# Optimization experiments

Hardware: AMD Instinct MI355X
Metric: run time of the kernel (lower is better)

## Reference

```python
import jax, jax.numpy as jnp
import numpy as np

B, T = 32, 512
D_TOK, D_OH, D_DEP = 256, 32, 32
D = D_TOK + D_OH + D_DEP  # tree_input_size = 320
H = 64                    # tree_lstm_h_size
P, L, ROOT = 16384, 16, 8 # pairs, path length, root position on path
N = P * L
E = P * (L - 1)
NUM_LEVELS = 9            # max level = max(ROOT, L-1-ROOT) = 8 -> levels 0..8


def _structure():
    # Each subgraph is a shortest path in the dependency tree; edges on both
    # sides point toward the topological root (position ROOT).
    pos = np.arange(L)
    par = np.where(pos < ROOT, pos + 1, np.where(pos > ROOT, pos - 1, pos))
    base = (np.arange(P) * L)[:, None]
    parent_of = (base + par[None, :]).reshape(-1).astype(np.int32)
    nodes = (base + pos[None, :]).reshape(-1).astype(np.int32)
    is_root = np.tile(pos == ROOT, P)
    child = nodes[~is_root]
    parent = parent_of[~is_root]
    level_up = np.tile(np.where(pos <= ROOT, pos, L - 1 - pos), P).astype(np.int32)
    level_down = np.tile(np.abs(pos - ROOT), P).astype(np.int32)
    root_idx = (np.arange(P) * L + ROOT).astype(np.int32)
    start_idx = (np.arange(P) * L).astype(np.int32)
    end_idx = (np.arange(P) * L + (L - 1)).astype(np.int32)
    return child, parent, parent_of, level_up, level_down, root_idx, start_idx, end_idx


def setup_inputs() -> dict:
    key = jax.random.key(0)
    ks = jax.random.split(key, 24)
    sc = 0.02
    ch, pa, po, lu, ld, ri, si, ei = _structure()
    inp = {
        'token_embs': jax.random.normal(ks[0], (B, T, D_TOK), jnp.float32),
        'one_hot_embs': (jax.random.uniform(ks[1], (B, T, D_OH)) < 0.1).astype(jnp.float32),
        'dep_embs': jax.random.normal(ks[2], (B, T, D_DEP), jnp.float32),
        'node_b_idx': jax.random.randint(ks[3], (N,), 0, B, jnp.int32),
        'node_t_idx': jax.random.randint(ks[4], (N,), 0, T, jnp.int32),
        'child': jnp.asarray(ch), 'parent': jnp.asarray(pa),
        'parent_of': jnp.asarray(po),
        'level_up': jnp.asarray(lu), 'level_down': jnp.asarray(ld),
        'root_idx': jnp.asarray(ri), 'start_idx': jnp.asarray(si), 'end_idx': jnp.asarray(ei),
        # child-sum Tree-LSTM params, upward (bottom-up) direction
        'W_iou_up': jax.random.normal(ks[5], (D, 3 * H)) * sc,
        'U_iou_up': jax.random.normal(ks[6], (H, 3 * H)) * sc,
        'b_iou_up': jnp.zeros((3 * H,), jnp.float32),
        'W_f_up': jax.random.normal(ks[7], (D, H)) * sc,
        'U_f_up': jax.random.normal(ks[8], (H, H)) * sc,
        'b_f_up': jnp.zeros((H,), jnp.float32),
        # downward (top-down) direction
        'W_iou_dn': jax.random.normal(ks[9], (D, 3 * H)) * sc,
        'U_iou_dn': jax.random.normal(ks[10], (H, 3 * H)) * sc,
        'b_iou_dn': jnp.zeros((3 * H,), jnp.float32),
        'W_f_dn': jax.random.normal(ks[11], (D, H)) * sc,
        'U_f_dn': jax.random.normal(ks[12], (H, H)) * sc,
        'b_f_dn': jnp.zeros((H,), jnp.float32),
    }
    return inp


def _tree_lstm(x, child, parent, level, x_iou, x_f, U_iou, U_f):
    # Level-synchronous child-sum Tree-LSTM toward parents (bottom-up).
    n = x.shape[0]
    h0 = jnp.zeros((n, H), x.dtype)
    c0 = jnp.zeros((n, H), x.dtype)

    def step(carry, t):
        h, c = carry
        hs = jax.ops.segment_sum(h[child], parent, num_segments=n)          # sum child h
        f = jax.nn.sigmoid(x_f[parent] + h[child] @ U_f)                    # per-edge forget
        fc = jax.ops.segment_sum(f * c[child], parent, num_segments=n)
        i, o, u = jnp.split(x_iou + hs @ U_iou, 3, axis=-1)
        c_new = jax.nn.sigmoid(i) * jnp.tanh(u) + fc
        h_new = jax.nn.sigmoid(o) * jnp.tanh(c_new)
        m = (level == t)[:, None]
        return (jnp.where(m, h_new, h), jnp.where(m, c_new, c)), None

    (h, c), _ = jax.lax.scan(step, (h0, c0), jnp.arange(NUM_LEVELS))
    return h


def _tree_lstm_down(x, parent_of, level_down, x_iou, x_f, U_iou, U_f):
    # Top-down pass: each node has exactly one predecessor (its parent).
    n = x.shape[0]
    not_root = (level_down != 0).astype(x.dtype)[:, None]
    h0 = jnp.zeros((n, H), x.dtype)
    c0 = jnp.zeros((n, H), x.dtype)

    def step(carry, t):
        h, c = carry
        hp = h[parent_of] * not_root
        cp = c[parent_of] * not_root
        f = jax.nn.sigmoid(x_f + hp @ U_f)
        i, o, u = jnp.split(x_iou + hp @ U_iou, 3, axis=-1)
        c_new = jax.nn.sigmoid(i) * jnp.tanh(u) + f * cp
        h_new = jax.nn.sigmoid(o) * jnp.tanh(c_new)
        m = (level_down == t)[:, None]
        return (jnp.where(m, h_new, h), jnp.where(m, c_new, c)), None

    (h, c), _ = jax.lax.scan(step, (h0, c0), jnp.arange(NUM_LEVELS))
    return h


def reference(token_embs, one_hot_embs, dep_embs, node_b_idx, node_t_idx,
              child, parent, parent_of, level_up, level_down,
              root_idx, start_idx, end_idx,
              W_iou_up, U_iou_up, b_iou_up, W_f_up, U_f_up, b_f_up,
              W_iou_dn, U_iou_dn, b_iou_dn, W_f_dn, U_f_dn, b_f_dn):
    # node_embs = cat(token, one_hot, dep) gathered at subgraph node ids (_ID)
    full = jnp.concatenate((token_embs, one_hot_embs, dep_embs), axis=-1)  # [B,T,D]
    x = full[node_b_idx, node_t_idx]                                       # [N,D]

    # precompute input projections once
    xi_u = x @ W_iou_up + b_iou_up
    xf_u = x @ W_f_up + b_f_up
    xi_d = x @ W_iou_dn + b_iou_dn
    xf_d = x @ W_f_dn + b_f_dn

    h_up = _tree_lstm(x, child, parent, level_up, xi_u, xf_u, U_iou_up, U_f_up)
    h_dn = _tree_lstm_down(x, parent_of, level_down, xi_d, xf_d, U_iou_dn, U_f_dn)

    # tree_lstm_out.view(-1,2,H): slot 0 = bottom-up, slot 1 = top-down
    tree_pair_embs = jnp.concatenate(
        (h_up[root_idx], h_dn[start_idx], h_dn[end_idx]), axis=-1)          # [P, 3H]
    return tree_pair_embs
```

## Files before the change

### kernel.cpp

```cpp
#include <hip/hip_runtime.h>
#include <hip/hip_fp16.h>


typedef _Float16 f16x8 __attribute__((ext_vector_type(8)));
typedef _Float16 f16x4 __attribute__((ext_vector_type(4)));
typedef _Float16 f16x2 __attribute__((ext_vector_type(2)));
typedef float f32x4 __attribute__((ext_vector_type(4)));

#define NP 16
#define N2K 2.8853900817779268f

__device__ __forceinline__ void async16(const void* g, void* l) {
    __builtin_amdgcn_global_load_lds(
        (const __attribute__((address_space(1))) void*)g,
        (__attribute__((address_space(3))) void*)l, 16, 0, 0);
}
__device__ __forceinline__ void lgkm_barrier() {
    asm volatile("s_waitcnt lgkmcnt(0)\n\ts_barrier" ::: "memory");
}
__device__ __forceinline__ f32x4 exp2v(f32x4 x) {
    f32x4 y;
    y[0] = __builtin_amdgcn_exp2f(x[0]);
    y[1] = __builtin_amdgcn_exp2f(x[1]);
    y[2] = __builtin_amdgcn_exp2f(x[2]);
    y[3] = __builtin_amdgcn_exp2f(x[3]);
    return y;
}
__device__ __forceinline__ f32x4 rcpv(f32x4 x) {
    f32x4 y;
    y[0] = __builtin_amdgcn_rcpf(x[0]);
    y[1] = __builtin_amdgcn_rcpf(x[1]);
    y[2] = __builtin_amdgcn_rcpf(x[2]);
    y[3] = __builtin_amdgcn_rcpf(x[3]);
    return y;
}

__global__ __launch_bounds__(256) void prep_kernel(
    const float* __restrict__ Wi_u, const float* __restrict__ Ui_u,
    const float* __restrict__ bi_u, const float* __restrict__ Wf_u,
    const float* __restrict__ Uf_u, const float* __restrict__ bf_u,
    const float* __restrict__ Wi_d, const float* __restrict__ Ui_d,
    const float* __restrict__ bi_d, const float* __restrict__ Wf_d,
    const float* __restrict__ Uf_d, const float* __restrict__ bf_d,
    _Float16* __restrict__ Bx, _Float16* __restrict__ Upk,
    float* __restrict__ pb)
{
    int idx = blockIdx.x * 256 + threadIdx.x;
    if (idx < 512) {
        int d = idx >> 8, c = idx & 255, u = c >> 2, g = c & 3;
        const float* bio = d ? bi_d : bi_u;
        const float* bf  = d ? bf_d : bf_u;
        float s = (g == 2) ? -N2K : -0.5f * N2K;
        pb[idx] = s * ((g < 3) ? bio[g * 64 + u] : bf[u]);
    }
    if (idx < 163840) {
        int d = idx / 81920, r1 = idx % 81920;
        int c = r1 / 320, k = r1 % 320, u = c >> 2, g = c & 3;
        const float* Wio = d ? Wi_d : Wi_u;
        const float* Wf  = d ? Wf_d : Wf_u;
        float s = (g == 2) ? -N2K : -0.5f * N2K;
        Bx[idx] = (_Float16)(s * ((g < 3) ? Wio[k * 192 + g * 64 + u]
                                          : Wf[k * 64 + u]));
    } else {
        int j = idx - 163840;
        int d = j >> 14, r2 = j & 16383;
        int g = r2 >> 12, u = (r2 >> 6) & 63, k = r2 & 63;
        const float* Uio = d ? Ui_d : Ui_u;
        const float* Uf  = d ? Uf_d : Uf_u;
        float s = (g == 2) ? -N2K : -0.5f * N2K;
        Upk[j] = (_Float16)(s * ((g < 3) ? Uio[k * 192 + g * 64 + u]
                                         : Uf[k * 64 + u]));
    }
}

__global__ __launch_bounds__(256, 2) void xp_gemm(
    const float* __restrict__ tok, const float* __restrict__ oh,
    const float* __restrict__ dep,
    const _Float16* __restrict__ Bx, const float* __restrict__ pb,
    _Float16* __restrict__ XP)
{
    __shared__ _Float16 At[32 * 64];
    __shared__ _Float16 Btl[256 * 64];
    const int dir = blockIdx.x & 1, mt = blockIdx.x >> 1;
    const int tid = threadIdx.x, lane = tid & 63, w = tid >> 6;
    const int l15 = lane & 15, qd = lane >> 4;
    const int rsub = lane >> 3, pg = lane & 7;
    const int kg = (pg - rsub) & 7;
    const int koff = kg * 8;
    const int rowbase = mt * 32;
    const _Float16* Bb = Bx + (size_t)dir * 81920 + (w * 64 + rsub) * 320 + koff;

    f32x4 acc[2][4];
    #pragma unroll
    for (int i = 0; i < 2; ++i)
        #pragma unroll
        for (int j = 0; j < 4; ++j) acc[i][j] = (f32x4){0.f, 0.f, 0.f, 0.f};

    #pragma unroll
    for (int kt = 0; kt < 5; ++kt) {
        {
            int row = rowbase + w * 8 + rsub;
            int g = kt * 8 + kg;
            const float* src = (g < 32) ? tok + (size_t)row * 256 + g * 8
                             : (g < 36) ? oh  + (size_t)row * 32 + (g - 32) * 8
                                        : dep + (size_t)row * 32 + (g - 36) * 8;
            float4 f0 = *(const float4*)src;
            float4 f1 = *(const float4*)(src + 4);
            f16x8 v;
            v[0] = (_Float16)f0.x; v[1] = (_Float16)f0.y;
            v[2] = (_Float16)f0.z; v[3] = (_Float16)f0.w;
            v[4] = (_Float16)f1.x; v[5] = (_Float16)f1.y;
            v[6] = (_Float16)f1.z; v[7] = (_Float16)f1.w;
            *(f16x8*)&At[(w * 8 + rsub) * 64 + pg * 8] = v;
        }
        #pragma unroll
        for (int is = 0; is < 8; ++is)
            async16(Bb + (size_t)is * 8 * 320 + kt * 64,
                    &Btl[(w * 64 + is * 8) * 64]);
        __syncthreads();
        #pragma unroll
        for (int s = 0; s < 2; ++s) {
            const int g0 = s * 4 + qd;
            f16x8 af[2];
            #pragma unroll
            for (int i = 0; i < 2; ++i) {
                int R = i * 16 + l15;
                af[i] = *(const f16x8*)&At[R * 64 + ((g0 + R) & 7) * 8];
            }
            #pragma unroll
            for (int j = 0; j < 4; ++j) {
                int C = j * 64 + w * 16 + l15;
                f16x8 bf = *(const f16x8*)&Btl[C * 64 + ((g0 + C) & 7) * 8];
                #pragma unroll
                for (int i = 0; i < 2; ++i)
                    acc[i][j] = __builtin_amdgcn_mfma_f32_16x16x32_f16(
                        af[i], bf, acc[i][j], 0, 0, 0);
            }
        }
        __syncthreads();
    }
    #pragma unroll
    for (int i = 0; i < 2; ++i)
        #pragma unroll
        for (int j = 0; j < 4; ++j) {
            int colp = j * 64 + w * 16 + l15;
            float bias = pb[dir * 256 + colp];
            #pragma unroll
            for (int r = 0; r < 4; ++r) {
                int row = rowbase + i * 16 + qd * 4 + r;
                XP[(size_t)row * 512 + dir * 256 + colp] =
                    (_Float16)(acc[i][j][r] + bias);
            }
        }
}

template<int RPP>
__device__ __forceinline__ void gather_xp(
    const char* __restrict__ XPd, const int (*btl)[NP],
    int p0, int p1, int unit, int qd, f16x4* px)
{
    #pragma unroll
    for (int i = 0; i < RPP; ++i)
        #pragma unroll
        for (int r = 0; r < 4; ++r) {
            int row = i * 16 + qd * 4 + r;
            int pl  = (RPP == 2) ? (row >> 1) : row;
            int pos = (RPP == 2) ? ((row & 1) ? p1 : p0) : p0;
            px[i * 4 + r] = *(const f16x4*)(XPd + btl[pos][pl] + unit * 8);
        }
}

template<int RPP>
__device__ __forceinline__ void side_level(
    const f16x8 (*bfr)[4], const f16x4* px,
    const _Float16 (*hR)[68], const _Float16 (*cR)[68],
    _Float16 (*hW)[68], _Float16 (*cWl)[68],
    f16x2* crR, f16x2* crW, int cregr, int cwEn,
    float* __restrict__ out, int pair0,
    int rs0, int rs1, int oc0, int oc1,
    int unit, int l15, int qd)
{
    f32x4 acc[RPP][4];
    #pragma unroll
    for (int i = 0; i < RPP; ++i)
        #pragma unroll
        for (int r = 0; r < 4; ++r) {
            f16x4 g4 = px[i * 4 + r];
            acc[i][0][r] = (float)g4[0];
            acc[i][1][r] = (float)g4[1];
            acc[i][2][r] = (float)g4[2];
            acc[i][3][r] = (float)g4[3];
        }

    if (rs0 >= 0) {
        #pragma unroll
        for (int s = 0; s < 2; ++s)
            #pragma unroll
            for (int i = 0; i < RPP; ++i) {
                int R = i * 16 + l15;
                int arow = (RPP == 2) ? ((R & ~1) | ((R & 1) ? rs1 : rs0))
                                      : (R * 2 + rs0);
                f16x8 af = *(const f16x8*)&hR[arow][s * 32 + qd * 8];
                #pragma unroll
                for (int g = 0; g < 4; ++g)
                    acc[i][g] = __builtin_amdgcn_mfma_f32_16x16x32_f16(
                        af, bfr[s][g], acc[i][g], 0, 0, 0);
            }
    }

    #pragma unroll
    for (int i = 0; i < RPP; ++i) {
        f32x4 CIN;
        #pragma unroll
        for (int r = 0; r < 4; ++r) {
            int row = i * 16 + qd * 4 + r;
            int pl   = (RPP == 2) ? (row >> 1) : row;
            int slot = (RPP == 2) ? (row & 1) : 0;
            int rs = slot ? rs1 : rs0;
            if (RPP == 2 && cregr)
                CIN[r] = (float)crR[i * 2 + (r >> 1)][rs];
            else
                CIN[r] = (rs >= 0) ? (float)cR[pl * 2 + rs][unit] : 0.f;
        }
        f32x4 EA = exp2v(acc[i][0]);
        f32x4 EO = exp2v(acc[i][1]);
        f32x4 EB = exp2v(acc[i][2]);
        f32x4 EC = exp2v(acc[i][3]);
        f32x4 PQ = (1.f + EA) * (1.f + EB);
        f32x4 PC = 1.f + EC;
        f32x4 NUM = CIN * PQ + (1.f - EB) * PC;
        f32x4 CN = NUM * rcpv(PQ * PC);
        f32x4 EE = exp2v(-N2K * CN);
        f32x4 H = (1.f - EE) * rcpv((1.f + EE) * (1.f + EO));
        #pragma unroll
        for (int r = 0; r < 4; ++r) {
            int row = i * 16 + qd * 4 + r;
            int pl   = (RPP == 2) ? (row >> 1) : row;
            int slot = (RPP == 2) ? (row & 1) : 0;
            int oc = slot ? oc1 : oc0;
            if (oc >= 0) {
                out[(size_t)(pair0 + pl) * 192 + oc + unit] = H[r];
            } else {
                hW[pl * 2 + slot][unit] = (_Float16)H[r];
                if (cwEn) cWl[pl * 2 + slot][unit] = (_Float16)CN[r];
                if (RPP == 2) crW[i * 2 + (r >> 1)][r & 1] = (_Float16)CN[r];
            }
        }
    }
}

__device__ __forceinline__ void root_level(
    const f16x8 (*bfr)[4], const f16x4* px,
    const _Float16 (*hR0)[68], const _Float16 (*cR0)[68],
    const _Float16 (*hR1)[68], const _Float16 (*cR1)[68],
    float* __restrict__ out, int pair0, int unit, int l15, int qd)
{
    f32x4 aio[3], aF7, aF9;
    #pragma unroll
    for (int r = 0; r < 4; ++r) {
        f16x4 g4 = px[r];
        aio[0][r] = (float)g4[0];
        aio[1][r] = (float)g4[1];
        aio[2][r] = (float)g4[2];
        aF7[r] = (float)g4[3];
        aF9[r] = (float)g4[3];
    }
    #pragma unroll
    for (int s = 0; s < 2; ++s) {
        f16x8 v7 = *(const f16x8*)&hR0[l15 * 2 + 0][s * 32 + qd * 8];
        f16x8 v9 = *(const f16x8*)&hR1[l15 * 2 + 1][s * 32 + qd * 8];
        f16x8 vs = v7 + v9;
        aio[0] = __builtin_amdgcn_mfma_f32_16x16x32_f16(vs, bfr[s][0], aio[0], 0, 0, 0);
        aio[1] = __builtin_amdgcn_mfma_f32_16x16x32_f16(vs, bfr[s][1], aio[1], 0, 0, 0);
        aio[2] = __builtin_amdgcn_mfma_f32_16x16x32_f16(vs, bfr[s][2], aio[2], 0, 0, 0);
        aF7 = __builtin_amdgcn_mfma_f32_16x16x32_f16(v7, bfr[s][3], aF7, 0, 0, 0);
        aF9 = __builtin_amdgcn_mfma_f32_16x16x32_f16(v9, bfr[s][3], aF9, 0, 0, 0);
    }
    f32x4 C7, C9;
    #pragma unroll
    for (int r = 0; r < 4; ++r) {
        int pl = qd * 4 + r;
        C7[r] = (float)cR0[pl * 2 + 0][unit];
        C9[r] = (float)cR1[pl * 2 + 1][unit];
    }
    f32x4 EA = exp2v(aio[0]);
    f32x4 EO = exp2v(aio[1]);
    f32x4 EB = exp2v(aio[2]);
    f32x4 E7 = exp2v(aF7);
    f32x4 E9 = exp2v(aF9);
    f32x4 PQ  = (1.f + EA) * (1.f + EB);
    f32x4 S7  = 1.f + E7, S9 = 1.f + E9;
    f32x4 S79 = S7 * S9;
    f32x4 NUM = PQ * (C7 * S9 + C9 * S7) + (1.f - EB) * S79;
    f32x4 CN  = NUM * rcpv(PQ * S79);
    f32x4 EE  = exp2v(-N2K * CN);
    f32x4 H   = (1.f - EE) * rcpv((1.f + EE) * (1.f + EO));
    #pragma unroll
    for (int r = 0; r < 4; ++r) {
        int pl = qd * 4 + r;
        out[(size_t)(pair0 + pl) * 192 + unit] = H[r];
    }
}

__global__ __launch_bounds__(256, 2) void tree_kernel(
    const int* __restrict__ nb, const int* __restrict__ nt,
    const _Float16* __restrict__ XP, const _Float16* __restrict__ Upk,
    float* __restrict__ out)
{
    __shared__ _Float16 hS[2][2][NP * 2][68];
    __shared__ _Float16 cS[2][2][NP * 2][68];
    __shared__ int btl[16][NP];

    const int tid = threadIdx.x, lane = tid & 63, w = tid >> 6;
    const int l15 = lane & 15, qd = lane >> 4;
    const int unit = w * 16 + l15;
    const int pair0 = blockIdx.x * NP;

    {
        int pos = tid >> 4, pl = tid & 15;
        int node = (pair0 + pl) * 16 + pos;
        btl[pos][pl] = (nb[node] * 512 + nt[node]) * 1024;
    }

    f16x8 bU[2][4], bD[2][4];
    #pragma unroll
    for (int s = 0; s < 2; ++s)
        #pragma unroll
        for (int g = 0; g < 4; ++g) {
            bU[s][g] = *(const f16x8*)(Upk + (g * 64 + unit) * 64 + s * 32 + qd * 8);
            bD[s][g] = *(const f16x8*)(Upk + 16384 + (g * 64 + unit) * 64 + s * 32 + qd * 8);
        }

    __syncthreads();

    const char* XPu = (const char*)XP;
    const char* XPdn = XPu + 512;

    f16x2 creg[2][2][4] = {};

    f16x4 pxu[3][8], pxd[8];
    gather_xp<2>(XPu, btl, 0, 15, unit, qd, pxu[0]);
    gather_xp<2>(XPu, btl, 1, 14, unit, qd, pxu[1]);

    #pragma unroll
    for (int t = 0; t < 9; ++t) {
        const int pt = t & 1, pw = pt ^ 1;
        const int cur = t % 3, nx2 = (t + 2) % 3;
        if (t == 0)      gather_xp<1>(XPdn, btl, 8, 8, unit, qd, pxd);
        else if (t == 8) gather_xp<1>(XPdn, btl, 0, 0, unit, qd, pxd);
        else             gather_xp<2>(XPdn, btl, 8 - t, 8 + t, unit, qd, pxd);
        if (t < 5)       gather_xp<2>(XPu, btl, t + 2, 13 - t, unit, qd, pxu[nx2]);
        else if (t == 5) gather_xp<1>(XPu, btl, 7, 7, unit, qd, pxu[nx2]);
        else if (t == 6) gather_xp<1>(XPu, btl, 8, 8, unit, qd, pxu[nx2]);

        if (t < 7)
            side_level<2>(bU, pxu[cur], hS[pt][0], cS[pt][0],
                          hS[pw][0], cS[pw][0],
                          creg[pt][0], creg[pw][0],
                          (t >= 1) ? 1 : 0, (t == 6) ? 1 : 0,
                          out, pair0,
                          t ? 0 : -1, t ? 1 : -1, -1, -1, unit, l15, qd);
        else if (t == 7)
            side_level<1>(bU, pxu[cur], hS[pt][0], cS[pt][0],
                          hS[pw][0], cS[pw][0],
                          creg[pt][0], creg[pw][0], 0, 1,
                          out, pair0,
                          0, 0, -1, -1, unit, l15, qd);
        else
            root_level(bU, pxu[cur], hS[0][0], cS[0][0], hS[1][0], cS[1][0],
                       out, pair0, unit, l15, qd);

        if (t == 0)
            side_level<1>(bD, pxd, hS[pt][1], cS[pt][1],
                          hS[pw][1], cS[pw][1],
                          creg[pt][1], creg[pw][1], 0, 1,
                          out, pair0,
                          -1, -1, -1, -1, unit, l15, qd);
        else if (t == 8)
            side_level<1>(bD, pxd, hS[pt][1], cS[pt][1],
                          hS[pw][1], cS[pw][1],
                          creg[pt][1], creg[pw][1], 0, 0,
                          out, pair0,
                          0, 0, 64, 64, unit, l15, qd);
        else
            side_level<2>(bD, pxd, hS[pt][1], cS[pt][1],
                          hS[pw][1], cS[pw][1],
                          creg[pt][1], creg[pw][1],
                          (t >= 2) ? 1 : 0, (t == 7) ? 1 : 0,
                          out, pair0,
                          0, (t == 1) ? 0 : 1, -1, (t == 7) ? 128 : -1,
                          unit, l15, qd);

        lgkm_barrier();
    }
}

extern "C" void kernel_launch(void* const* d_in, const int* in_sizes, int n_in,
                              void* d_out, int out_size, void* d_ws, size_t ws_size,
                              hipStream_t stream)
{
    const float* tok  = (const float*)d_in[0];
    const float* ohp  = (const float*)d_in[1];
    const float* dep  = (const float*)d_in[2];
    const int*   nb   = (const int*)d_in[3];
    const int*   nt   = (const int*)d_in[4];
    const float* Wi_u = (const float*)d_in[13];
    const float* Ui_u = (const float*)d_in[14];
    const float* bi_u = (const float*)d_in[15];
    const float* Wf_u = (const float*)d_in[16];
    const float* Uf_u = (const float*)d_in[17];
    const float* bf_u = (const float*)d_in[18];
    const float* Wi_d = (const float*)d_in[19];
    const float* Ui_d = (const float*)d_in[20];
    const float* bi_d = (const float*)d_in[21];
    const float* Wf_d = (const float*)d_in[22];
    const float* Uf_d = (const float*)d_in[23];
    const float* bf_d = (const float*)d_in[24];

    char* ws = (char*)d_ws;
    _Float16* Bx  = (_Float16*)(ws);
    _Float16* Upk = (_Float16*)(ws + 0x50000);
    float*    pb  = (float*)   (ws + 0x60000);
    _Float16* XP  = (_Float16*)(ws + (12u << 20));
    float* out = (float*)d_out;

    prep_kernel<<<768, 256, 0, stream>>>(Wi_u, Ui_u, bi_u, Wf_u, Uf_u, bf_u,
                                         Wi_d, Ui_d, bi_d, Wf_d, Uf_d, bf_d,
                                         Bx, Upk, pb);
    xp_gemm<<<1024, 256, 0, stream>>>(tok, ohp, dep, Bx, pb, XP);
    tree_kernel<<<1024, 256, 0, stream>>>(nb, nt, XP, Upk, out);

    (void)in_sizes; (void)n_in; (void)out_size; (void)ws_size;
}
```

Before: 184.9 us.

## Split up and down tree passes into separate blocks to double grid parallelism

Each block now handles only one direction (bottom-up or top-down) for its 16 pairs, selected by the low bit of the block index, and the grid doubles to 2048 blocks. Shared memory, U-weight registers and gather buffers are halved per block, which should allow more resident blocks and more parallel work across CUs. The cost is that node index loading is duplicated across the two blocks per pair group, and the interleaving of two independent chains inside one block, which hid latency, is lost.

```diff
diff --git a/kernel.cpp b/kernel.cpp
--- a/kernel.cpp
+++ b/kernel.cpp
@@ -307,14 +307,15 @@
     const _Float16* __restrict__ XP, const _Float16* __restrict__ Upk,
     float* __restrict__ out)
 {
-    __shared__ _Float16 hS[2][2][NP * 2][68];
-    __shared__ _Float16 cS[2][2][NP * 2][68];
+    __shared__ _Float16 hS[2][NP * 2][68];
+    __shared__ _Float16 cS[2][NP * 2][68];
     __shared__ int btl[16][NP];
 
     const int tid = threadIdx.x, lane = tid & 63, w = tid >> 6;
     const int l15 = lane & 15, qd = lane >> 4;
     const int unit = w * 16 + l15;
-    const int pair0 = blockIdx.x * NP;
+    const int side = blockIdx.x & 1;
+    const int pair0 = (blockIdx.x >> 1) * NP;
 
     {
         int pos = tid >> 4, pl = tid & 15;
@@ -322,76 +323,70 @@
         btl[pos][pl] = (nb[node] * 512 + nt[node]) * 1024;
     }
 
-    f16x8 bU[2][4], bD[2][4];
+    f16x8 bfr[2][4];
     #pragma unroll
     for (int s = 0; s < 2; ++s)
         #pragma unroll
-        for (int g = 0; g < 4; ++g) {
-            bU[s][g] = *(const f16x8*)(Upk + (g * 64 + unit) * 64 + s * 32 + qd * 8);
-            bD[s][g] = *(const f16x8*)(Upk + 16384 + (g * 64 + unit) * 64 + s * 32 + qd * 8);
-        }
+        for (int g = 0; g < 4; ++g)
+            bfr[s][g] = *(const f16x8*)(Upk + side * 16384 +
+                          (g * 64 + unit) * 64 + s * 32 + qd * 8);
 
     __syncthreads();
 
-    const char* XPu = (const char*)XP;
-    const char* XPdn = XPu + 512;
-
-    f16x2 creg[2][2][4] = {};
-
-    f16x4 pxu[3][8], pxd[8];
-    gather_xp<2>(XPu, btl, 0, 15, unit, qd, pxu[0]);
-    gather_xp<2>(XPu, btl, 1, 14, unit, qd, pxu[1]);
-
-    #pragma unroll
-    for (int t = 0; t < 9; ++t) {
-        const int pt = t & 1, pw = pt ^ 1;
-        const int cur = t % 3, nx2 = (t + 2) % 3;
-        if (t == 0)      gather_xp<1>(XPdn, btl, 8, 8, unit, qd, pxd);
-        else if (t == 8) gather_xp<1>(XPdn, btl, 0, 0, unit, qd, pxd);
-        else             gather_xp<2>(XPdn, btl, 8 - t, 8 + t, unit, qd, pxd);
-        if (t < 5)       gather_xp<2>(XPu, btl, t + 2, 13 - t, unit, qd, pxu[nx2]);
-        else if (t == 5) gather_xp<1>(XPu, btl, 7, 7, unit, qd, pxu[nx2]);
-        else if (t == 6) gather_xp<1>(XPu, btl, 8, 8, unit, qd, pxu[nx2]);
-
-        if (t < 7)
-            side_level<2>(bU, pxu[cur], hS[pt][0], cS[pt][0],
-                          hS[pw][0], cS[pw][0],
-                          creg[pt][0], creg[pw][0],
-                          (t >= 1) ? 1 : 0, (t == 6) ? 1 : 0,
-                          out, pair0,
-                          t ? 0 : -1, t ? 1 : -1, -1, -1, unit, l15, qd);
-        else if (t == 7)
-            side_level<1>(bU, pxu[cur], hS[pt][0], cS[pt][0],
-                          hS[pw][0], cS[pw][0],
-                          creg[pt][0], creg[pw][0], 0, 1,
-                          out, pair0,
-                          0, 0, -1, -1, unit, l15, qd);
-        else
-            root_level(bU, pxu[cur], hS[0][0], cS[0][0], hS[1][0], cS[1][0],
-                       out, pair0, unit, l15, qd);
-
-        if (t == 0)
-            side_level<1>(bD, pxd, hS[pt][1], cS[pt][1],
-                          hS[pw][1], cS[pw][1],
-                          creg[pt][1], creg[pw][1], 0, 1,
-                          out, pair0,
-                          -1, -1, -1, -1, unit, l15, qd);
-        else if (t == 8)
-            side_level<1>(bD, pxd, hS[pt][1], cS[pt][1],
-                          hS[pw][1], cS[pw][1],
-                          creg[pt][1], creg[pw][1], 0, 0,
-                          out, pair0,
-                          0, 0, 64, 64, unit, l15, qd);
-        else
-            side_level<2>(bD, pxd, hS[pt][1], cS[pt][1],
-                          hS[pw][1], cS[pw][1],
-                          creg[pt][1], creg[pw][1],
-                          (t >= 2) ? 1 : 0, (t == 7) ? 1 : 0,
-                          out, pair0,
-                          0, (t == 1) ? 0 : 1, -1, (t == 7) ? 128 : -1,
-                          unit, l15, qd);
-
-        lgkm_barrier();
+    const char* XPs = (const char*)XP + side * 512;
+
+    f16x2 creg[2][4] = {};
+    f16x4 px[2][8];
+
+    if (side == 0) {
+        gather_xp<2>(XPs, btl, 0, 15, unit, qd, px[0]);
+        #pragma unroll
+        for (int t = 0; t < 9; ++t) {
+            const int pt = t & 1, pw = pt ^ 1;
+            if (t < 6)       gather_xp<2>(XPs, btl, t + 1, 14 - t, unit, qd, px[pw]);
+            else if (t == 6) gather_xp<1>(XPs, btl, 7, 7, unit, qd, px[pw]);
+            else if (t == 7) gather_xp<1>(XPs, btl, 8, 8, unit, qd, px[pw]);
+
+            if (t < 7)
+                side_level<2>(bfr, px[pt], hS[pt], cS[pt], hS[pw], cS[pw],
+                              creg[pt], creg[pw],
+                              (t >= 1) ? 1 : 0, (t == 6) ? 1 : 0,
+                              out, pair0,
+                              t ? 0 : -1, t ? 1 : -1, -1, -1, unit, l15, qd);
+            else if (t == 7)
+                side_level<1>(bfr, px[pt], hS[pt], cS[pt], hS[pw], cS[pw],
+                              creg[pt], creg[pw], 0, 1,
+                              out, pair0, 0, 0, -1, -1, unit, l15, qd);
+            else
+                root_level(bfr, px[pt], hS[0], cS[0], hS[1], cS[1],
+                           out, pair0, unit, l15, qd);
+            lgkm_barrier();
+        }
+    } else {
+        gather_xp<1>(XPs, btl, 8, 8, unit, qd, px[0]);
+        #pragma unroll
+        for (int t = 0; t < 9; ++t) {
+            const int pt = t & 1, pw = pt ^ 1;
+            if (t < 7)       gather_xp<2>(XPs, btl, 7 - t, 9 + t, unit, qd, px[pw]);
+            else if (t == 7) gather_xp<1>(XPs, btl, 0, 0, unit, qd, px[pw]);
+
+            if (t == 0)
+                side_level<1>(bfr, px[pt], hS[pt], cS[pt], hS[pw], cS[pw],
+                              creg[pt], creg[pw], 0, 1,
+                              out, pair0, -1, -1, -1, -1, unit, l15, qd);
+            else if (t == 8)
+                side_level<1>(bfr, px[pt], hS[pt], cS[pt], hS[pw], cS[pw],
+                              creg[pt], creg[pw], 0, 0,
+                              out, pair0, 0, 0, 64, 64, unit, l15, qd);
+            else
+                side_level<2>(bfr, px[pt], hS[pt], cS[pt], hS[pw], cS[pw],
+                              creg[pt], creg[pw],
+                              (t >= 2) ? 1 : 0, (t == 7) ? 1 : 0,
+                              out, pair0,
+                              0, (t == 1) ? 0 : 1, -1, (t == 7) ? 128 : -1,
+                              unit, l15, qd);
+            lgkm_barrier();
+        }
     }
 }
 
@@ -428,7 +423,7 @@
                                          Wi_d, Ui_d, bi_d, Wf_d, Uf_d, bf_d,
                                          Bx, Upk, pb);
     xp_gemm<<<1024, 256, 0, stream>>>(tok, ohp, dep, Bx, pb, XP);
-    tree_kernel<<<1024, 256, 0, stream>>>(nb, nt, XP, Upk, out);
+    tree_kernel<<<2048, 256, 0, stream>>>(nb, nt, XP, Upk, out);
 
     (void)in_sizes; (void)n_in; (void)out_size; (void)ws_size;
 }
```

Result: faster. 178.2 us (median of 2 runs) (-3.6%).
